# Optimization experiments

Measured on AMD Instinct MI355X. Metric: run time of the kernel, lower is better.

The kernel has to match this reference:

```python
import jax, jax.numpy as jnp
import numpy as np
import math

NUM_HEADS = 16
KEY_SIZE = 64
HIDDEN = 4096
EMBED = 1024
VOCAB = 32000
SEQ = 2048
LAYERS = 4


def rmsnorm(x):
    return x * jax.lax.rsqrt(jnp.mean(x * x, axis=-1, keepdims=True) + 1e-5)


def rope_buffers(seq, d):
    half = d // 2
    i = jnp.arange(d)
    offset = i % half
    scales = jnp.power(10000.0, (-2.0 / d) * offset.astype(jnp.float32))
    m = jnp.arange(seq, dtype=jnp.float32)
    angles = m[:, None] * scales[None, :]  # [S, D]
    cos = jnp.cos(angles)
    sin = jnp.sin(angles)
    sin = jnp.concatenate([-sin[:, :half], sin[:, half:]], axis=-1)
    return cos, sin


def rotate(x, cos, sin):
    # x: [B, H, S, D]; cos/sin: [S, D]
    half = KEY_SIZE // 2
    swapped = jnp.concatenate([x[..., half:], x[..., :half]], axis=-1)
    return cos[None, None] * x + sin[None, None] * swapped


def setup_inputs() -> dict:
    key = jax.random.key(0)
    ks = jax.random.split(key, 7)
    std = 0.02
    return {
        'tokens': jax.random.randint(ks[0], (1, SEQ), 0, VOCAB),
        'table': jax.random.normal(ks[1], (VOCAB, EMBED), jnp.float32) * std,
        'qkv_w': jax.random.normal(ks[2], (LAYERS, EMBED, 3 * NUM_HEADS * KEY_SIZE), jnp.float32) * std,
        'out_w': jax.random.normal(ks[3], (LAYERS, NUM_HEADS * KEY_SIZE, EMBED), jnp.float32) * std,
        'up_w': jax.random.normal(ks[4], (LAYERS, EMBED, 2 * HIDDEN), jnp.float32) * std,
        'down_w': jax.random.normal(ks[5], (LAYERS, HIDDEN, EMBED), jnp.float32) * std,
        'vocab_w': jax.random.normal(ks[6], (EMBED, VOCAB), jnp.float32) * std,
    }


def reference(tokens, table, qkv_w, out_w, up_w, down_w, vocab_w):
    B, S = tokens.shape
    H, D = NUM_HEADS, KEY_SIZE
    # module zeroes embedding row 0 each forward
    table = table.at[0].set(0.0)
    cos, sin = rope_buffers(S, D)
    causal = jnp.tril(jnp.ones((S, S), dtype=bool))  # context_size == S -> pure causal
    emb = table[tokens]  # [B, S, E]
    for l in range(LAYERS):
        # --- self attention ---
        normed = rmsnorm(emb)
        qkv = normed @ qkv_w[l]  # [B, S, 3HD]
        q, k, v = jnp.split(qkv, 3, axis=-1)
        q = q.reshape(B, S, H, D).transpose(0, 2, 1, 3)
        k = k.reshape(B, S, H, D).transpose(0, 2, 1, 3)
        v = v.reshape(B, S, H, D).transpose(0, 2, 1, 3)
        q = rotate(q, cos, sin)
        k = rotate(k, cos, sin)
        attn = jnp.einsum('bhqd,bhkd->bhqk', q, k) / math.sqrt(D)
        attn = jnp.where(causal[None, None], attn, -jnp.inf)
        attn = jax.nn.softmax(attn, axis=-1)
        out = jnp.einsum('bhqk,bhkd->bhqd', attn, v)
        out = out.transpose(0, 2, 1, 3).reshape(B, S, H * D)
        emb = emb + out @ out_w[l]
        # --- SwiGLU FFN ---
        normed = rmsnorm(emb)
        gate_up = normed @ up_w[l]
        gate, up = gate_up[..., :HIDDEN], gate_up[..., HIDDEN:]
        emb = emb + (up * jax.nn.silu(gate)) @ down_w[l]
    emb = rmsnorm(emb)
    logits = emb @ vocab_w  # [B, S, V]
    return logits
```

## Files before the change

### kernel.cpp

```cpp
#include <hip/hip_runtime.h>
#include <hip/hip_bf16.h>

typedef __attribute__((ext_vector_type(8))) short short8;
typedef __attribute__((ext_vector_type(4))) float f32x4;

__device__ __forceinline__ ushort f2bf(float f) {
  uint32_t u = __float_as_uint(f);
  uint32_t r = (u + 0x7FFFu + ((u >> 16) & 1u)) >> 16;
  return (ushort)r;
}
__device__ __forceinline__ float bf2f(ushort u) {
  return __uint_as_float(((uint32_t)u) << 16);
}

__device__ __forceinline__ void gload_lds16(const ushort* g, ushort* l) {
  __builtin_amdgcn_global_load_lds(
      (const __attribute__((address_space(1))) void*)g,
      (__attribute__((address_space(3))) void*)l, 16, 0, 0);
}

__device__ __forceinline__ f32x4 mfma16(short8 a, short8 b, f32x4 c) {
  return __builtin_amdgcn_mfma_f32_16x16x32_bf16(a, b, c, 0, 0, 0);
}

#define BAR() __builtin_amdgcn_s_barrier()
#define WAIT_LGKM()                                        \
  do {                                                     \
    asm volatile("s_waitcnt lgkmcnt(0)" ::: "memory");     \
    __builtin_amdgcn_sched_barrier(0);                     \
  } while (0)
#define WAIT_VM()                                          \
  do {                                                     \
    asm volatile("s_waitcnt vmcnt(0)" ::: "memory");       \
    __builtin_amdgcn_sched_barrier(0);                     \
  } while (0)

__global__ __launch_bounds__(256)
void transpose_conv_kernel(const float* __restrict__ W, ushort* __restrict__ WT,
                           const int K, const int N, const int mode) {
  const size_t lofs = (size_t)blockIdx.z * K * N;
  W += lofs;
  WT += lofs;
  __shared__ float tile[32][33];
  const int n0 = blockIdx.x * 32;
  const int k0 = blockIdx.y * 32;
  const int x = threadIdx.x;
  const int y = threadIdx.y;
#pragma unroll
  for (int j = 0; j < 4; ++j)
    tile[y + j * 8][x] = W[(size_t)(k0 + y + j * 8) * N + n0 + x];
  __syncthreads();
#pragma unroll
  for (int j = 0; j < 4; ++j) {
    int r = n0 + y + j * 8;
    if (mode == 1) r = (r < 4096) ? (2 * r) : (2 * (r - 4096) + 1);
    WT[(size_t)r * K + k0 + x] = f2bf(tile[x][y + j * 8]);
  }
}

__global__ __launch_bounds__(256)
void embed_kernel(const int* __restrict__ tokens, const float* __restrict__ table,
                  float* __restrict__ emb) {
  const int s = blockIdx.x, t = threadIdx.x;
  const int tok = tokens[s];
  float4 v = make_float4(0.f, 0.f, 0.f, 0.f);
  if (tok != 0) v = *(const float4*)&table[(size_t)tok * 1024 + t * 4];
  *(float4*)&emb[(size_t)s * 1024 + t * 4] = v;
}

__global__ __launch_bounds__(256)
void rmsnorm_kernel(const float* __restrict__ x, ushort* __restrict__ out) {
  const int row = blockIdx.x, t = threadIdx.x;
  const float4 v = *(const float4*)&x[(size_t)row * 1024 + t * 4];
  float ss = v.x * v.x + v.y * v.y + v.z * v.z + v.w * v.w;
#pragma unroll
  for (int off = 32; off; off >>= 1) ss += __shfl_xor(ss, off);
  __shared__ float red[4];
  if ((t & 63) == 0) red[t >> 6] = ss;
  __syncthreads();
  const float total = red[0] + red[1] + red[2] + red[3];
  const float sc = rsqrtf(total * (1.f / 1024.f) + 1e-5f);
  ushort4 o;
  o.x = f2bf(v.x * sc); o.y = f2bf(v.y * sc);
  o.z = f2bf(v.z * sc); o.w = f2bf(v.w * sc);
  *(ushort4*)&out[(size_t)row * 1024 + t * 4] = o;
}

__global__ __launch_bounds__(256)
void ropev_kernel(const float* __restrict__ qkv, ushort* __restrict__ qh,
                  ushort* __restrict__ kh, ushort* __restrict__ vt) {
  __shared__ float tv[64][65];
  const int h = blockIdx.y;
  const int s0 = blockIdx.x * 64;
  const int t = threadIdx.x;
#pragma unroll
  for (int j = 0; j < 4; ++j) {
    const int e = j * 1024 + t * 4;
    const int sl = e >> 6, d0 = e & 63;
    const int s = s0 + sl;
    const float* row = qkv + (size_t)s * 3072 + h * 64;
    const float4 xq  = *(const float4*)&row[d0];
    const float4 xqs = *(const float4*)&row[(d0 + 32) & 63];
    const float4 xk  = *(const float4*)&row[1024 + d0];
    const float4 xks = *(const float4*)&row[1024 + ((d0 + 32) & 63)];
    const float4 xv  = *(const float4*)&row[2048 + d0];
    float co[4], si[4];
#pragma unroll
    for (int c = 0; c < 4; ++c) {
      const int d = d0 + c;
      const int off = d & 31;
      const float freq = exp2f(-0.41524101186092029f * (float)off);
      const float ang = (float)s * freq;
      co[c] = cosf(ang);
      const float sv = sinf(ang);
      si[c] = (d < 32) ? -sv : sv;
    }
    ushort4 oq, ok;
    oq.x = f2bf(co[0] * xq.x + si[0] * xqs.x);
    oq.y = f2bf(co[1] * xq.y + si[1] * xqs.y);
    oq.z = f2bf(co[2] * xq.z + si[2] * xqs.z);
    oq.w = f2bf(co[3] * xq.w + si[3] * xqs.w);
    ok.x = f2bf(co[0] * xk.x + si[0] * xks.x);
    ok.y = f2bf(co[1] * xk.y + si[1] * xks.y);
    ok.z = f2bf(co[2] * xk.z + si[2] * xks.z);
    ok.w = f2bf(co[3] * xk.w + si[3] * xks.w);
    const size_t ho = ((size_t)h * 2048 + s) * 64 + d0;
    *(ushort4*)&qh[ho] = oq;
    *(ushort4*)&kh[ho] = ok;
    *(float4*)&tv[sl][d0] = xv;
  }
  __syncthreads();
#pragma unroll
  for (int j = 0; j < 4; ++j) {
    const int e = j * 1024 + t * 4;
    const int d = e >> 6, s4 = e & 63;
    ushort4 ov;
    ov.x = f2bf(tv[s4 + 0][d]);
    ov.y = f2bf(tv[s4 + 1][d]);
    ov.z = f2bf(tv[s4 + 2][d]);
    ov.w = f2bf(tv[s4 + 3][d]);
    *(ushort4*)&vt[((size_t)h * 64 + d) * 2048 + s0 + s4] = ov;
  }
}

__global__ __launch_bounds__(256)
void attn_mfma_kernel(const ushort* __restrict__ qh, const ushort* __restrict__ kh,
                      const ushort* __restrict__ vt, ushort* __restrict__ attn_out) {
  __shared__ ushort sQ[64 * 64];
  __shared__ ushort sK[64 * 64];
  __shared__ ushort sV[64 * 64];
  __shared__ ushort sP[4][1024];
  const int h = blockIdx.y;
  const int bx = blockIdx.x;
  const int qt = (h < 8) ? bx : 31 - bx;
  const int i0 = qt * 64;
  const int tid = threadIdx.x;
  const int w = tid >> 6, lane = tid & 63;
  const int llo = lane & 15, lhi = lane >> 4;
  const int lr = lane >> 3, lc = lane & 7;
  const ushort* qg = qh + ((size_t)h * 2048 + i0) * 64;
  const ushort* kg = kh + (size_t)h * 2048 * 64;
  const ushort* vg = vt + (size_t)h * 64 * 2048;

#pragma unroll
  for (int j = 0; j < 2; ++j) {
    const int r0 = (w * 2 + j) * 8;
    const int row = r0 + lr;
    gload_lds16(qg + (size_t)row * 64 + ((lc ^ (row & 7)) * 8), &sQ[r0 * 64]);
  }
  __syncthreads();
  const int qrow = w * 16 + llo;
  const short8 qf0 = *(const short8*)&sQ[qrow * 64 + ((lhi ^ (qrow & 7)) * 8)];
  const short8 qf1 = *(const short8*)&sQ[qrow * 64 + (((4 + lhi) ^ (qrow & 7)) * 8)];

  float m = -1e30f, lsum = 0.f;
  f32x4 o[4] = {};
  const int nch = qt + 1;
  for (int cb = 0; cb < nch; ++cb) {
    const int kb = cb * 64;
    __syncthreads();
#pragma unroll
    for (int j = 0; j < 2; ++j) {
      const int r0 = (w * 2 + j) * 8;
      const int row = r0 + lr;
      gload_lds16(kg + (size_t)(kb + row) * 64 + ((lc ^ (row & 7)) * 8), &sK[r0 * 64]);
      gload_lds16(vg + (size_t)row * 2048 + kb + ((lc ^ (row & 7)) * 8), &sV[r0 * 64]);
    }
    __syncthreads();

    f32x4 st[4] = {};
#pragma unroll
    for (int ck = 0; ck < 2; ++ck) {
      const short8 qf = ck ? qf1 : qf0;
#pragma unroll
      for (int f = 0; f < 4; ++f) {
        const int key = f * 16 + llo;
        const short8 kf = *(const short8*)&sK[key * 64 + (((ck * 4 + lhi) ^ (key & 7)) * 8)];
        st[f] = mfma16(kf, qf, st[f]);
      }
    }

    float pv[4][4];
    const bool diag = (kb == i0);
#pragma unroll
    for (int f = 0; f < 4; ++f)
#pragma unroll
      for (int r = 0; r < 4; ++r) {
        float x = st[f][r] * 0.125f;
        if (diag && (f * 16 + lhi * 4 + r) > qrow) x = -1e30f;
        pv[f][r] = x;
      }
    float mr = pv[0][0];
#pragma unroll
    for (int f = 0; f < 4; ++f)
#pragma unroll
      for (int r = 0; r < 4; ++r) mr = fmaxf(mr, pv[f][r]);
    mr = fmaxf(mr, __shfl_xor(mr, 16));
    mr = fmaxf(mr, __shfl_xor(mr, 32));
    const float mnew = fmaxf(m, mr);
    const float scale = __expf(m - mnew);
    m = mnew;
    float rs = 0.f;
#pragma unroll
    for (int f = 0; f < 4; ++f)
#pragma unroll
      for (int r = 0; r < 4; ++r) {
        const float p = __expf(pv[f][r] - mnew);
        pv[f][r] = p;
        rs += p;
      }
    rs += __shfl_xor(rs, 16);
    rs += __shfl_xor(rs, 32);
    lsum = lsum * scale + rs;
    float scr[4];
#pragma unroll
    for (int r = 0; r < 4; ++r) scr[r] = __shfl(scale, lhi * 4 + r);
#pragma unroll
    for (int nn = 0; nn < 4; ++nn)
#pragma unroll
      for (int r = 0; r < 4; ++r) o[nn][r] *= scr[r];

    ushort* pw = sP[w];
#pragma unroll
    for (int f = 0; f < 4; ++f) {
      uint2 pk;
      pk.x = (uint)f2bf(pv[f][0]) | ((uint)f2bf(pv[f][1]) << 16);
      pk.y = (uint)f2bf(pv[f][2]) | ((uint)f2bf(pv[f][3]) << 16);
      *(uint2*)&pw[llo * 64 + ((f * 16 + lhi * 4) ^ ((llo & 7) << 3))] = pk;
    }
    const short8 pf0 = *(const short8*)&pw[llo * 64 + ((lhi ^ (llo & 7)) * 8)];
    const short8 pf1 = *(const short8*)&pw[llo * 64 + (((4 + lhi) ^ (llo & 7)) * 8)];

#pragma unroll
    for (int ck = 0; ck < 2; ++ck) {
      const short8 pf = ck ? pf1 : pf0;
#pragma unroll
      for (int nn = 0; nn < 4; ++nn) {
        const int drow = nn * 16 + llo;
        const short8 vf = *(const short8*)&sV[drow * 64 + (((ck * 4 + lhi) ^ (drow & 7)) * 8)];
        o[nn] = mfma16(pf, vf, o[nn]);
      }
    }
  }

  const float inv = 1.f / lsum;
  float invr[4];
#pragma unroll
  for (int r = 0; r < 4; ++r) invr[r] = __shfl(inv, lhi * 4 + r);
#pragma unroll
  for (int nn = 0; nn < 4; ++nn)
#pragma unroll
    for (int r = 0; r < 4; ++r) {
      const int row = i0 + w * 16 + lhi * 4 + r;
      attn_out[(size_t)row * 1024 + h * 64 + nn * 16 + llo] = f2bf(o[nn][r] * invr[r]);
    }
}

template <int BM, int BN, int EPI>
__global__ __launch_bounds__(256)
void gemm_bt_kernel(const ushort* __restrict__ A, const ushort* __restrict__ BT,
                    const float* __restrict__ addend, void* __restrict__ Cout,
                    const int M, const int N, const int K) {
  constexpr int WM = BM / 2, WN = BN / 2;
  constexpr int FM = WM / 16, FN = WN / 16;
  constexpr int CHA = BM / 16, CHB = BN / 16;
  __shared__ ushort sA[BM * 32];
  __shared__ ushort sB[BN * 32];
  const int bm0 = blockIdx.y * BM;
  const int bn0 = blockIdx.x * BN;
  const int tid = threadIdx.x;
  const int wid = tid >> 6;
  const int lane = tid & 63;
  const int wr = wid >> 1, wc = wid & 1;
  const int lhi = lane >> 4, llo = lane & 15;
  f32x4 acc[FM][FN] = {};
  for (int kt = 0; kt < K; kt += 32) {
#pragma unroll
    for (int c2 = 0; c2 < CHA / 4; ++c2) {
      const int ch = c2 * 4 + wid;
      const int e = ch * 512 + lane * 8;
      gload_lds16(A + (size_t)(bm0 + (e >> 5)) * K + kt + (e & 31), sA + ch * 512);
    }
#pragma unroll
    for (int c2 = 0; c2 < CHB / 4; ++c2) {
      const int ch = c2 * 4 + wid;
      const int e = ch * 512 + lane * 8;
      gload_lds16(BT + (size_t)(bn0 + (e >> 5)) * K + kt + (e & 31), sB + ch * 512);
    }
    __syncthreads();
    short8 aF[FM], bF[FN];
#pragma unroll
    for (int mm = 0; mm < FM; ++mm)
      aF[mm] = *(const short8*)&sA[(wr * WM + mm * 16 + llo) * 32 + lhi * 8];
#pragma unroll
    for (int nn = 0; nn < FN; ++nn)
      bF[nn] = *(const short8*)&sB[(wc * WN + nn * 16 + llo) * 32 + lhi * 8];
#pragma unroll
    for (int mm = 0; mm < FM; ++mm)
#pragma unroll
      for (int nn = 0; nn < FN; ++nn)
        acc[mm][nn] = __builtin_amdgcn_mfma_f32_16x16x32_bf16(aF[mm], bF[nn],
                                                              acc[mm][nn], 0, 0, 0);
    __syncthreads();
  }
#pragma unroll
  for (int mm = 0; mm < FM; ++mm) {
#pragma unroll
    for (int nn = 0; nn < FN; ++nn) {
      const int col = bn0 + wc * WN + nn * 16 + llo;
#pragma unroll
      for (int r = 0; r < 4; ++r) {
        const int row = bm0 + wr * WM + mm * 16 + lhi * 4 + r;
        float v = acc[mm][nn][r];
        if constexpr (EPI == 1) v += addend[(size_t)row * N + col];
        ((float*)Cout)[(size_t)row * N + col] = v;
      }
    }
  }
}

#define LDA_(MH)                                                              \
  {                                                                           \
    _Pragma("unroll") for (int mm = 0; mm < 4; ++mm) {                        \
      const int row = wr * 128 + ((MH) * 4 + mm) * 16 + llo;                  \
      _Pragma("unroll") for (int ks = 0; ks < 2; ++ks)                        \
          aF[mm][ks] = *(const short8*)&cA[row * 64 +                         \
                          (((ks * 4 + lhi) ^ (row & 7)) * 8)];                \
    }                                                                         \
  }
#define LDB_(NH)                                                              \
  {                                                                           \
    _Pragma("unroll") for (int nn = 0; nn < 2; ++nn) {                        \
      const int row = wc * 64 + ((NH) * 2 + nn) * 16 + llo;                   \
      _Pragma("unroll") for (int ks = 0; ks < 2; ++ks)                        \
          bF[nn][ks] = *(const short8*)&cB[row * 64 +                         \
                          (((ks * 4 + lhi) ^ (row & 7)) * 8)];                \
    }                                                                         \
  }
#define MFMAQ_(MH, NH)                                                        \
  {                                                                           \
    __builtin_amdgcn_s_setprio(1);                                            \
    _Pragma("unroll") for (int mm = 0; mm < 4; ++mm)                          \
        _Pragma("unroll") for (int nn = 0; nn < 2; ++nn)                      \
            _Pragma("unroll") for (int ks = 0; ks < 2; ++ks)                  \
                acc[(MH) * 4 + mm][(NH) * 2 + nn] =                           \
                    mfma16(aF[mm][ks], bF[nn][ks],                            \
                           acc[(MH) * 4 + mm][(NH) * 2 + nn]);                \
    __builtin_amdgcn_s_setprio(0);                                            \
  }

template <int EPI>
__global__ __launch_bounds__(512, 2)
void gemm8_kernel(const ushort* __restrict__ A, const ushort* __restrict__ BT,
                  void* __restrict__ Cout,
                  const int M, const int N, const int K, const int nby) {
  extern __shared__ ushort smem[];
  const int nwg = gridDim.x;
  const int cpx = nwg >> 3;
  int id = blockIdx.x;
  id = (id & 7) * cpx + (id >> 3);
  const int by = id % nby, bx = id / nby;
  const int bm0 = by * 256, bn0 = bx * 256;
  const int tid = threadIdx.x;
  const int wid = tid >> 6, lane = tid & 63;
  const int wr = wid >> 2, wc = wid & 3;
  const int llo = lane & 15, lhi = lane >> 4;
  const ushort* gA = A + (size_t)bm0 * K;
  const ushort* gB = BT + (size_t)bn0 * K;

  auto stage = [&](const ushort* g, ushort* dst, int kt) {
#pragma unroll
    for (int i = 0; i < 4; ++i) {
      const int chunk = i * 512 + wid * 64 + lane;
      const int row = chunk >> 3, c = chunk & 7;
      gload_lds16(g + (size_t)row * K + kt + ((c ^ (row & 7)) * 8),
                  dst + (size_t)(i * 512 + wid * 64) * 8);
    }
  };

  f32x4 acc[8][4] = {};
  short8 aF[4][2];
  short8 bF[2][2];

  stage(gA, smem, 0);
  stage(gB, smem + 16384, 0);
  WAIT_VM();
  BAR();

  const int nt = K >> 6;
  for (int t = 0; t < nt; ++t) {
    const int cur = t & 1;
    ushort* cA = smem + cur * 32768;
    ushort* cB = cA + 16384;
    ushort* nA = smem + (cur ^ 1) * 32768;
    ushort* nB = nA + 16384;
    const bool pf = (t + 1 < nt);
    LDA_(0); LDB_(0);
    if (pf) { stage(gA, nA, (t + 1) * 64); stage(gB, nB, (t + 1) * 64); }
    BAR(); WAIT_LGKM();
    MFMAQ_(0, 0);
    BAR();
    LDB_(1);
    BAR(); WAIT_LGKM();
    MFMAQ_(0, 1);
    BAR();
    LDA_(1);
    BAR(); WAIT_LGKM();
    MFMAQ_(1, 1);
    BAR();
    LDB_(0);
    BAR(); WAIT_LGKM();
    MFMAQ_(1, 0);
    if (pf) WAIT_VM();
    BAR();
  }

#pragma unroll
  for (int m = 0; m < 8; ++m) {
#pragma unroll
    for (int n = 0; n < 4; ++n) {
      const int col = bn0 + wc * 64 + n * 16 + llo;
#pragma unroll
      for (int r = 0; r < 4; ++r) {
        const int row = bm0 + wr * 128 + m * 16 + lhi * 4 + r;
        float v = acc[m][n][r];
        if constexpr (EPI == 3) {
          const float other = __shfl_xor(v, 1);
          if ((llo & 1) == 0) {
            const float gate = v, up = other;
            const float hh = up * gate / (1.f + expf(-gate));
            ((ushort*)Cout)[(size_t)row * (N >> 1) + (col >> 1)] = f2bf(hh);
          }
        } else {
          ((float*)Cout)[(size_t)row * N + col] = v;
        }
      }
    }
  }
}

extern "C" void kernel_launch(void* const* d_in, const int* in_sizes, int n_in,
                              void* d_out, int out_size, void* d_ws, size_t ws_size,
                              hipStream_t stream) {
  const int* tokens    = (const int*)d_in[0];
  const float* table   = (const float*)d_in[1];
  const float* qkv_w   = (const float*)d_in[2];
  const float* out_w   = (const float*)d_in[3];
  const float* up_w    = (const float*)d_in[4];
  const float* down_w  = (const float*)d_in[5];
  const float* vocab_w = (const float*)d_in[6];
  float* logits = (float*)d_out;

  constexpr int G8_LDS = 131072;
  hipFuncSetAttribute(reinterpret_cast<const void*>(&gemm8_kernel<0>),
                      hipFuncAttributeMaxDynamicSharedMemorySize, G8_LDS);
  hipFuncSetAttribute(reinterpret_cast<const void*>(&gemm8_kernel<3>),
                      hipFuncAttributeMaxDynamicSharedMemorySize, G8_LDS);

  char* p = (char*)d_ws;
  auto alloc = [&](size_t bytes) {
    char* r = p;
    p += (bytes + 255) & ~(size_t)255;
    return r;
  };
  float*  emb    = (float*)alloc(2048ull * 1024 * 4);
  ushort* normed = (ushort*)alloc(2048ull * 1024 * 2);
  float*  qkvbuf = (float*)alloc(2048ull * 3072 * 4);
  ushort* qhb    = (ushort*)alloc(16ull * 2048 * 64 * 2);
  ushort* khb    = (ushort*)alloc(16ull * 2048 * 64 * 2);
  ushort* vtb    = (ushort*)alloc(16ull * 64 * 2048 * 2);
  ushort* attno  = (ushort*)alloc(2048ull * 1024 * 2);
  ushort* hbuf   = (ushort*)alloc(2048ull * 4096 * 2);
  ushort* qkvT   = (ushort*)alloc(4ull * 3072 * 1024 * 2);
  ushort* outT   = (ushort*)alloc(4ull * 1024 * 1024 * 2);
  ushort* upT    = (ushort*)alloc(4ull * 8192 * 1024 * 2);
  ushort* downT  = (ushort*)alloc(4ull * 1024 * 4096 * 2);
  ushort* vocabT = (ushort*)alloc(32000ull * 1024 * 2);

  const dim3 tb(32, 8);
  transpose_conv_kernel<<<dim3(3072 / 32, 1024 / 32, 4), tb, 0, stream>>>(
      qkv_w, qkvT, 1024, 3072, 0);
  transpose_conv_kernel<<<dim3(1024 / 32, 1024 / 32, 4), tb, 0, stream>>>(
      out_w, outT, 1024, 1024, 0);
  transpose_conv_kernel<<<dim3(8192 / 32, 1024 / 32, 4), tb, 0, stream>>>(
      up_w, upT, 1024, 8192, 1);
  transpose_conv_kernel<<<dim3(1024 / 32, 4096 / 32, 4), tb, 0, stream>>>(
      down_w, downT, 4096, 1024, 0);
  transpose_conv_kernel<<<dim3(32000 / 32, 1024 / 32, 1), tb, 0, stream>>>(
      vocab_w, vocabT, 1024, 32000, 0);

  embed_kernel<<<2048, 256, 0, stream>>>(tokens, table, emb);

  for (int l = 0; l < 4; ++l) {
    rmsnorm_kernel<<<2048, 256, 0, stream>>>(emb, normed);
    gemm_bt_kernel<64, 128, 0><<<dim3(3072 / 128, 2048 / 64), 256, 0, stream>>>(
        normed, qkvT + (size_t)l * 3072 * 1024, nullptr, qkvbuf, 2048, 3072, 1024);
    ropev_kernel<<<dim3(32, 16), 256, 0, stream>>>(qkvbuf, qhb, khb, vtb);
    attn_mfma_kernel<<<dim3(32, 16), 256, 0, stream>>>(qhb, khb, vtb, attno);
    gemm_bt_kernel<64, 128, 1><<<dim3(1024 / 128, 2048 / 64), 256, 0, stream>>>(
        attno, outT + (size_t)l * 1024 * 1024, emb, emb, 2048, 1024, 1024);
    rmsnorm_kernel<<<2048, 256, 0, stream>>>(emb, normed);
    gemm8_kernel<3><<<(8192 / 256) * (2048 / 256), 512, G8_LDS, stream>>>(
        normed, upT + (size_t)l * 8192 * 1024, hbuf, 2048, 8192, 1024, 2048 / 256);
    gemm_bt_kernel<64, 128, 1><<<dim3(1024 / 128, 2048 / 64), 256, 0, stream>>>(
        hbuf, downT + (size_t)l * 1024 * 4096, emb, emb, 2048, 1024, 4096);
  }
  rmsnorm_kernel<<<2048, 256, 0, stream>>>(emb, normed);
  gemm8_kernel<0><<<(32000 / 256) * (2048 / 256), 512, G8_LDS, stream>>>(
      normed, vocabT, logits, 2048, 32000, 1024, 2048 / 256);
}
```

Baseline: 1.335 ms.

## Use 256x128 triple-buffered GEMM, route QKV through it, fuse embed with rmsnorm

Replaces the 256x256 double-buffered GEMM with a 256x128 tile that keeps three LDS stages and prefetches two K-steps ahead, waiting only for the older stage's loads (vmcnt(6)). This is meant to hide more global-load latency and double the workgroup count for the up-projection and vocab GEMMs. The QKV projection moves from the small-tile GEMM to this kernel. The first layer's rmsnorm is fused into the embedding kernel to save one launch and one pass over the activations. In exchange, the narrower N tile lowers arithmetic intensity per loaded A tile, and the larger LDS footprint (144 KB) limits residency to one block per CU.

```diff
diff --git a/kernel.cpp b/kernel.cpp
--- a/kernel.cpp
+++ b/kernel.cpp
@@ -29,9 +29,14 @@
     asm volatile("s_waitcnt lgkmcnt(0)" ::: "memory");     \
     __builtin_amdgcn_sched_barrier(0);                     \
   } while (0)
-#define WAIT_VM()                                          \
+#define WAIT_VM0()                                         \
   do {                                                     \
     asm volatile("s_waitcnt vmcnt(0)" ::: "memory");       \
+    __builtin_amdgcn_sched_barrier(0);                     \
+  } while (0)
+#define WAIT_VM6()                                         \
+  do {                                                     \
+    asm volatile("s_waitcnt vmcnt(6)" ::: "memory");       \
     __builtin_amdgcn_sched_barrier(0);                     \
   } while (0)
 
@@ -59,13 +64,25 @@
 }
 
 __global__ __launch_bounds__(256)
-void embed_kernel(const int* __restrict__ tokens, const float* __restrict__ table,
-                  float* __restrict__ emb) {
+void embed_norm_kernel(const int* __restrict__ tokens, const float* __restrict__ table,
+                       float* __restrict__ emb, ushort* __restrict__ normed) {
   const int s = blockIdx.x, t = threadIdx.x;
   const int tok = tokens[s];
   float4 v = make_float4(0.f, 0.f, 0.f, 0.f);
   if (tok != 0) v = *(const float4*)&table[(size_t)tok * 1024 + t * 4];
   *(float4*)&emb[(size_t)s * 1024 + t * 4] = v;
+  float ss = v.x * v.x + v.y * v.y + v.z * v.z + v.w * v.w;
+#pragma unroll
+  for (int off = 32; off; off >>= 1) ss += __shfl_xor(ss, off);
+  __shared__ float red[4];
+  if ((t & 63) == 0) red[t >> 6] = ss;
+  __syncthreads();
+  const float total = red[0] + red[1] + red[2] + red[3];
+  const float sc = rsqrtf(total * (1.f / 1024.f) + 1e-5f);
+  ushort4 o;
+  o.x = f2bf(v.x * sc); o.y = f2bf(v.y * sc);
+  o.z = f2bf(v.z * sc); o.w = f2bf(v.w * sc);
+  *(ushort4*)&normed[(size_t)s * 1024 + t * 4] = o;
 }
 
 __global__ __launch_bounds__(256)
@@ -339,48 +356,18 @@
   }
 }
 
-#define LDA_(MH)                                                              \
-  {                                                                           \
-    _Pragma("unroll") for (int mm = 0; mm < 4; ++mm) {                        \
-      const int row = wr * 128 + ((MH) * 4 + mm) * 16 + llo;                  \
-      _Pragma("unroll") for (int ks = 0; ks < 2; ++ks)                        \
-          aF[mm][ks] = *(const short8*)&cA[row * 64 +                         \
-                          (((ks * 4 + lhi) ^ (row & 7)) * 8)];                \
-    }                                                                         \
-  }
-#define LDB_(NH)                                                              \
-  {                                                                           \
-    _Pragma("unroll") for (int nn = 0; nn < 2; ++nn) {                        \
-      const int row = wc * 64 + ((NH) * 2 + nn) * 16 + llo;                   \
-      _Pragma("unroll") for (int ks = 0; ks < 2; ++ks)                        \
-          bF[nn][ks] = *(const short8*)&cB[row * 64 +                         \
-                          (((ks * 4 + lhi) ^ (row & 7)) * 8)];                \
-    }                                                                         \
-  }
-#define MFMAQ_(MH, NH)                                                        \
-  {                                                                           \
-    __builtin_amdgcn_s_setprio(1);                                            \
-    _Pragma("unroll") for (int mm = 0; mm < 4; ++mm)                          \
-        _Pragma("unroll") for (int nn = 0; nn < 2; ++nn)                      \
-            _Pragma("unroll") for (int ks = 0; ks < 2; ++ks)                  \
-                acc[(MH) * 4 + mm][(NH) * 2 + nn] =                           \
-                    mfma16(aF[mm][ks], bF[nn][ks],                            \
-                           acc[(MH) * 4 + mm][(NH) * 2 + nn]);                \
-    __builtin_amdgcn_s_setprio(0);                                            \
-  }
-
 template <int EPI>
 __global__ __launch_bounds__(512, 2)
-void gemm8_kernel(const ushort* __restrict__ A, const ushort* __restrict__ BT,
-                  void* __restrict__ Cout,
-                  const int M, const int N, const int K, const int nby) {
+void gemm8b_kernel(const ushort* __restrict__ A, const ushort* __restrict__ BT,
+                   void* __restrict__ Cout,
+                   const int M, const int N, const int K, const int nby) {
   extern __shared__ ushort smem[];
   const int nwg = gridDim.x;
   const int cpx = nwg >> 3;
   int id = blockIdx.x;
   id = (id & 7) * cpx + (id >> 3);
   const int by = id % nby, bx = id / nby;
-  const int bm0 = by * 256, bn0 = bx * 256;
+  const int bm0 = by * 256, bn0 = bx * 128;
   const int tid = threadIdx.x;
   const int wid = tid >> 6, lane = tid & 63;
   const int wr = wid >> 2, wc = wid & 3;
@@ -388,58 +375,90 @@
   const ushort* gA = A + (size_t)bm0 * K;
   const ushort* gB = BT + (size_t)bn0 * K;
 
-  auto stage = [&](const ushort* g, ushort* dst, int kt) {
+  auto stage = [&](ushort* dst, int kt) {
 #pragma unroll
     for (int i = 0; i < 4; ++i) {
       const int chunk = i * 512 + wid * 64 + lane;
       const int row = chunk >> 3, c = chunk & 7;
-      gload_lds16(g + (size_t)row * K + kt + ((c ^ (row & 7)) * 8),
+      gload_lds16(gA + (size_t)row * K + kt + ((c ^ (row & 7)) * 8),
                   dst + (size_t)(i * 512 + wid * 64) * 8);
     }
+#pragma unroll
+    for (int i = 0; i < 2; ++i) {
+      const int chunk = i * 512 + wid * 64 + lane;
+      const int row = chunk >> 3, c = chunk & 7;
+      gload_lds16(gB + (size_t)row * K + kt + ((c ^ (row & 7)) * 8),
+                  dst + 16384 + (size_t)(i * 512 + wid * 64) * 8);
+    }
   };
 
-  f32x4 acc[8][4] = {};
-  short8 aF[4][2];
-  short8 bF[2][2];
-
-  stage(gA, smem, 0);
-  stage(gB, smem + 16384, 0);
-  WAIT_VM();
+  f32x4 acc[8][2] = {};
+  short8 aF[8][2];
+  short8 bF[2];
+
+  const int nt = K >> 6;
+  stage(smem, 0);
+  if (nt > 1) {
+    stage(smem + 24576, 64);
+    WAIT_VM6();
+  } else {
+    WAIT_VM0();
+  }
   BAR();
 
-  const int nt = K >> 6;
+  int cs = 0;
   for (int t = 0; t < nt; ++t) {
-    const int cur = t & 1;
-    ushort* cA = smem + cur * 32768;
+    ushort* cA = smem + cs * 24576;
     ushort* cB = cA + 16384;
-    ushort* nA = smem + (cur ^ 1) * 32768;
-    ushort* nB = nA + 16384;
-    const bool pf = (t + 1 < nt);
-    LDA_(0); LDB_(0);
-    if (pf) { stage(gA, nA, (t + 1) * 64); stage(gB, nB, (t + 1) * 64); }
+    int ss = cs + 2; if (ss >= 3) ss -= 3;
+    const bool pf2 = (t + 2 < nt);
+    if (pf2) stage(smem + ss * 24576, (t + 2) * 64);
+#pragma unroll
+    for (int mm = 0; mm < 8; ++mm) {
+      const int row = wr * 128 + mm * 16 + llo;
+#pragma unroll
+      for (int ks = 0; ks < 2; ++ks)
+        aF[mm][ks] = *(const short8*)&cA[row * 64 + (((ks * 4 + lhi) ^ (row & 7)) * 8)];
+    }
+    {
+      const int row = wc * 32 + llo;
+#pragma unroll
+      for (int ks = 0; ks < 2; ++ks)
+        bF[ks] = *(const short8*)&cB[row * 64 + (((ks * 4 + lhi) ^ (row & 7)) * 8)];
+    }
     BAR(); WAIT_LGKM();
-    MFMAQ_(0, 0);
+    __builtin_amdgcn_s_setprio(1);
+#pragma unroll
+    for (int mm = 0; mm < 8; ++mm)
+#pragma unroll
+      for (int ks = 0; ks < 2; ++ks)
+        acc[mm][0] = mfma16(aF[mm][ks], bF[ks], acc[mm][0]);
+    __builtin_amdgcn_s_setprio(0);
     BAR();
-    LDB_(1);
+    {
+      const int row = wc * 32 + 16 + llo;
+#pragma unroll
+      for (int ks = 0; ks < 2; ++ks)
+        bF[ks] = *(const short8*)&cB[row * 64 + (((ks * 4 + lhi) ^ (row & 7)) * 8)];
+    }
     BAR(); WAIT_LGKM();
-    MFMAQ_(0, 1);
+    __builtin_amdgcn_s_setprio(1);
+#pragma unroll
+    for (int mm = 0; mm < 8; ++mm)
+#pragma unroll
+      for (int ks = 0; ks < 2; ++ks)
+        acc[mm][1] = mfma16(aF[mm][ks], bF[ks], acc[mm][1]);
+    __builtin_amdgcn_s_setprio(0);
+    if (pf2) { WAIT_VM6(); } else { WAIT_VM0(); }
     BAR();
-    LDA_(1);
-    BAR(); WAIT_LGKM();
-    MFMAQ_(1, 1);
-    BAR();
-    LDB_(0);
-    BAR(); WAIT_LGKM();
-    MFMAQ_(1, 0);
-    if (pf) WAIT_VM();
-    BAR();
+    ++cs; if (cs == 3) cs = 0;
   }
 
 #pragma unroll
   for (int m = 0; m < 8; ++m) {
 #pragma unroll
-    for (int n = 0; n < 4; ++n) {
-      const int col = bn0 + wc * 64 + n * 16 + llo;
+    for (int n = 0; n < 2; ++n) {
+      const int col = bn0 + wc * 32 + n * 16 + llo;
 #pragma unroll
       for (int r = 0; r < 4; ++r) {
         const int row = bm0 + wr * 128 + m * 16 + lhi * 4 + r;
@@ -471,10 +490,10 @@
   const float* vocab_w = (const float*)d_in[6];
   float* logits = (float*)d_out;
 
-  constexpr int G8_LDS = 131072;
-  hipFuncSetAttribute(reinterpret_cast<const void*>(&gemm8_kernel<0>),
+  constexpr int G8_LDS = 147456;
+  hipFuncSetAttribute(reinterpret_cast<const void*>(&gemm8b_kernel<0>),
                       hipFuncAttributeMaxDynamicSharedMemorySize, G8_LDS);
-  hipFuncSetAttribute(reinterpret_cast<const void*>(&gemm8_kernel<3>),
+  hipFuncSetAttribute(reinterpret_cast<const void*>(&gemm8b_kernel<3>),
                       hipFuncAttributeMaxDynamicSharedMemorySize, G8_LDS);
 
   char* p = (char*)d_ws;
@@ -509,23 +528,23 @@
   transpose_conv_kernel<<<dim3(32000 / 32, 1024 / 32, 1), tb, 0, stream>>>(
       vocab_w, vocabT, 1024, 32000, 0);
 
-  embed_kernel<<<2048, 256, 0, stream>>>(tokens, table, emb);
+  embed_norm_kernel<<<2048, 256, 0, stream>>>(tokens, table, emb, normed);
 
   for (int l = 0; l < 4; ++l) {
-    rmsnorm_kernel<<<2048, 256, 0, stream>>>(emb, normed);
-    gemm_bt_kernel<64, 128, 0><<<dim3(3072 / 128, 2048 / 64), 256, 0, stream>>>(
-        normed, qkvT + (size_t)l * 3072 * 1024, nullptr, qkvbuf, 2048, 3072, 1024);
+    if (l > 0) rmsnorm_kernel<<<2048, 256, 0, stream>>>(emb, normed);
+    gemm8b_kernel<0><<<(3072 / 128) * (2048 / 256), 512, G8_LDS, stream>>>(
+        normed, qkvT + (size_t)l * 3072 * 1024, qkvbuf, 2048, 3072, 1024, 2048 / 256);
     ropev_kernel<<<dim3(32, 16), 256, 0, stream>>>(qkvbuf, qhb, khb, vtb);
     attn_mfma_kernel<<<dim3(32, 16), 256, 0, stream>>>(qhb, khb, vtb, attno);
     gemm_bt_kernel<64, 128, 1><<<dim3(1024 / 128, 2048 / 64), 256, 0, stream>>>(
         attno, outT + (size_t)l * 1024 * 1024, emb, emb, 2048, 1024, 1024);
     rmsnorm_kernel<<<2048, 256, 0, stream>>>(emb, normed);
-    gemm8_kernel<3><<<(8192 / 256) * (2048 / 256), 512, G8_LDS, stream>>>(
+    gemm8b_kernel<3><<<(8192 / 128) * (2048 / 256), 512, G8_LDS, stream>>>(
         normed, upT + (size_t)l * 8192 * 1024, hbuf, 2048, 8192, 1024, 2048 / 256);
     gemm_bt_kernel<64, 128, 1><<<dim3(1024 / 128, 2048 / 64), 256, 0, stream>>>(
         hbuf, downT + (size_t)l * 1024 * 4096, emb, emb, 2048, 1024, 4096);
   }
   rmsnorm_kernel<<<2048, 256, 0, stream>>>(emb, normed);
-  gemm8_kernel<0><<<(32000 / 256) * (2048 / 256), 512, G8_LDS, stream>>>(
+  gemm8b_kernel<0><<<(32000 / 128) * (2048 / 256), 512, G8_LDS, stream>>>(
       normed, vocabT, logits, 2048, 32000, 1024, 2048 / 256);
 }
```

Measured after the change: 1.333 ms. Within noise of the previous version (-0.1%).

## Fuse RoPE into QKV GEMM epilogue and widen weight-transpose tiles

Applied to the files above, without the earlier changes.

The QKV GEMM now applies rotary embedding in its epilogue, using a precomputed cos/sin table, and writes bf16 Q/K/V in per-head layout directly. This removes the fp32 qkv buffer round trip and the per-element transcendental math in the old rope kernel. A small kernel now only transposes V. Separately, the first layer's rmsnorm is fused into the embedding kernel, and the weight transpose-convert kernel uses 64x64 tiles with vectorized float4 loads and ushort4 stores. The epilogue stores are scattered 2-byte writes, which may be less coalesced.

```diff
diff --git a/kernel.cpp b/kernel.cpp
--- a/kernel.cpp
+++ b/kernel.cpp
@@ -29,7 +29,7 @@
     asm volatile("s_waitcnt lgkmcnt(0)" ::: "memory");     \
     __builtin_amdgcn_sched_barrier(0);                     \
   } while (0)
-#define WAIT_VM()                                          \
+#define WAIT_VM0()                                         \
   do {                                                     \
     asm volatile("s_waitcnt vmcnt(0)" ::: "memory");       \
     __builtin_amdgcn_sched_barrier(0);                     \
@@ -41,31 +41,61 @@
   const size_t lofs = (size_t)blockIdx.z * K * N;
   W += lofs;
   WT += lofs;
-  __shared__ float tile[32][33];
-  const int n0 = blockIdx.x * 32;
-  const int k0 = blockIdx.y * 32;
-  const int x = threadIdx.x;
-  const int y = threadIdx.y;
-#pragma unroll
-  for (int j = 0; j < 4; ++j)
-    tile[y + j * 8][x] = W[(size_t)(k0 + y + j * 8) * N + n0 + x];
+  __shared__ float tile[64][65];
+  const int n0 = blockIdx.x * 64;
+  const int k0 = blockIdx.y * 64;
+  const int t = threadIdx.x;
+#pragma unroll
+  for (int j = 0; j < 4; ++j) {
+    const int idx = j * 1024 + t * 4;
+    const int kk = idx >> 6, nn = idx & 63;
+    *(float4*)&tile[kk][nn] = *(const float4*)&W[(size_t)(k0 + kk) * N + n0 + nn];
+  }
   __syncthreads();
 #pragma unroll
   for (int j = 0; j < 4; ++j) {
-    int r = n0 + y + j * 8;
-    if (mode == 1) r = (r < 4096) ? (2 * r) : (2 * (r - 4096) + 1);
-    WT[(size_t)r * K + k0 + x] = f2bf(tile[x][y + j * 8]);
-  }
-}
-
-__global__ __launch_bounds__(256)
-void embed_kernel(const int* __restrict__ tokens, const float* __restrict__ table,
-                  float* __restrict__ emb) {
+    const int idx = j * 1024 + t * 4;
+    const int nn = idx >> 6, kk = idx & 63;
+    int rr = n0 + nn;
+    if (mode == 1) rr = (rr < 4096) ? (2 * rr) : (2 * (rr - 4096) + 1);
+    ushort4 o;
+    o.x = f2bf(tile[kk + 0][nn]);
+    o.y = f2bf(tile[kk + 1][nn]);
+    o.z = f2bf(tile[kk + 2][nn]);
+    o.w = f2bf(tile[kk + 3][nn]);
+    *(ushort4*)&WT[(size_t)rr * K + k0 + kk] = o;
+  }
+}
+
+__global__ __launch_bounds__(256)
+void sincos_kernel(float2* __restrict__ cstab) {
+  const int idx = blockIdx.x * 256 + threadIdx.x;
+  const int s = idx >> 5, o = idx & 31;
+  const float freq = exp2f(-0.41524101186092029f * (float)o);
+  const float a = (float)s * freq;
+  cstab[idx] = make_float2(cosf(a), sinf(a));
+}
+
+__global__ __launch_bounds__(256)
+void embed_norm_kernel(const int* __restrict__ tokens, const float* __restrict__ table,
+                       float* __restrict__ emb, ushort* __restrict__ normed) {
   const int s = blockIdx.x, t = threadIdx.x;
   const int tok = tokens[s];
   float4 v = make_float4(0.f, 0.f, 0.f, 0.f);
   if (tok != 0) v = *(const float4*)&table[(size_t)tok * 1024 + t * 4];
   *(float4*)&emb[(size_t)s * 1024 + t * 4] = v;
+  float ss = v.x * v.x + v.y * v.y + v.z * v.z + v.w * v.w;
+#pragma unroll
+  for (int off = 32; off; off >>= 1) ss += __shfl_xor(ss, off);
+  __shared__ float red[4];
+  if ((t & 63) == 0) red[t >> 6] = ss;
+  __syncthreads();
+  const float total = red[0] + red[1] + red[2] + red[3];
+  const float sc = rsqrtf(total * (1.f / 1024.f) + 1e-5f);
+  ushort4 o;
+  o.x = f2bf(v.x * sc); o.y = f2bf(v.y * sc);
+  o.z = f2bf(v.z * sc); o.w = f2bf(v.w * sc);
+  *(ushort4*)&normed[(size_t)s * 1024 + t * 4] = o;
 }
 
 __global__ __launch_bounds__(256)
@@ -87,58 +117,27 @@
 }
 
 __global__ __launch_bounds__(256)
-void ropev_kernel(const float* __restrict__ qkv, ushort* __restrict__ qh,
-                  ushort* __restrict__ kh, ushort* __restrict__ vt) {
-  __shared__ float tv[64][65];
+void vtrans_kernel(const ushort* __restrict__ vh, ushort* __restrict__ vt) {
+  __shared__ ushort tv[64][68];
   const int h = blockIdx.y;
   const int s0 = blockIdx.x * 64;
   const int t = threadIdx.x;
 #pragma unroll
   for (int j = 0; j < 4; ++j) {
-    const int e = j * 1024 + t * 4;
-    const int sl = e >> 6, d0 = e & 63;
-    const int s = s0 + sl;
-    const float* row = qkv + (size_t)s * 3072 + h * 64;
-    const float4 xq  = *(const float4*)&row[d0];
-    const float4 xqs = *(const float4*)&row[(d0 + 32) & 63];
-    const float4 xk  = *(const float4*)&row[1024 + d0];
-    const float4 xks = *(const float4*)&row[1024 + ((d0 + 32) & 63)];
-    const float4 xv  = *(const float4*)&row[2048 + d0];
-    float co[4], si[4];
-#pragma unroll
-    for (int c = 0; c < 4; ++c) {
-      const int d = d0 + c;
-      const int off = d & 31;
-      const float freq = exp2f(-0.41524101186092029f * (float)off);
-      const float ang = (float)s * freq;
-      co[c] = cosf(ang);
-      const float sv = sinf(ang);
-      si[c] = (d < 32) ? -sv : sv;
-    }
-    ushort4 oq, ok;
-    oq.x = f2bf(co[0] * xq.x + si[0] * xqs.x);
-    oq.y = f2bf(co[1] * xq.y + si[1] * xqs.y);
-    oq.z = f2bf(co[2] * xq.z + si[2] * xqs.z);
-    oq.w = f2bf(co[3] * xq.w + si[3] * xqs.w);
-    ok.x = f2bf(co[0] * xk.x + si[0] * xks.x);
-    ok.y = f2bf(co[1] * xk.y + si[1] * xks.y);
-    ok.z = f2bf(co[2] * xk.z + si[2] * xks.z);
-    ok.w = f2bf(co[3] * xk.w + si[3] * xks.w);
-    const size_t ho = ((size_t)h * 2048 + s) * 64 + d0;
-    *(ushort4*)&qh[ho] = oq;
-    *(ushort4*)&kh[ho] = ok;
-    *(float4*)&tv[sl][d0] = xv;
+    const int idx = j * 1024 + t * 4;
+    const int s = idx >> 6, d4 = idx & 63;
+    *(ushort4*)&tv[s][d4] = *(const ushort4*)&vh[((size_t)h * 2048 + s0 + s) * 64 + d4];
   }
   __syncthreads();
 #pragma unroll
   for (int j = 0; j < 4; ++j) {
-    const int e = j * 1024 + t * 4;
-    const int d = e >> 6, s4 = e & 63;
+    const int idx = j * 1024 + t * 4;
+    const int d = idx >> 6, s4 = idx & 63;
     ushort4 ov;
-    ov.x = f2bf(tv[s4 + 0][d]);
-    ov.y = f2bf(tv[s4 + 1][d]);
-    ov.z = f2bf(tv[s4 + 2][d]);
-    ov.w = f2bf(tv[s4 + 3][d]);
+    ov.x = tv[s4 + 0][d];
+    ov.y = tv[s4 + 1][d];
+    ov.z = tv[s4 + 2][d];
+    ov.w = tv[s4 + 3][d];
     *(ushort4*)&vt[((size_t)h * 64 + d) * 2048 + s0 + s4] = ov;
   }
 }
@@ -334,6 +333,79 @@
         float v = acc[mm][nn][r];
         if constexpr (EPI == 1) v += addend[(size_t)row * N + col];
         ((float*)Cout)[(size_t)row * N + col] = v;
+      }
+    }
+  }
+}
+
+__global__ __launch_bounds__(256)
+void gemm_qkv_kernel(const ushort* __restrict__ A, const ushort* __restrict__ BT,
+                     const float2* __restrict__ cstab, ushort* __restrict__ qh,
+                     ushort* __restrict__ kh, ushort* __restrict__ vh, const int K) {
+  constexpr int BM = 64, BN = 128, WM = 32, WN = 64, FM = 2, FN = 4;
+  constexpr int CHA = BM / 16, CHB = BN / 16;
+  __shared__ ushort sA[BM * 32];
+  __shared__ ushort sB[BN * 32];
+  const int bm0 = blockIdx.y * BM;
+  const int bn0 = blockIdx.x * BN;
+  const int tid = threadIdx.x;
+  const int wid = tid >> 6;
+  const int lane = tid & 63;
+  const int wr = wid >> 1, wc = wid & 1;
+  const int lhi = lane >> 4, llo = lane & 15;
+  f32x4 acc[FM][FN] = {};
+  for (int kt = 0; kt < K; kt += 32) {
+#pragma unroll
+    for (int c2 = 0; c2 < CHA / 4; ++c2) {
+      const int ch = c2 * 4 + wid;
+      const int e = ch * 512 + lane * 8;
+      gload_lds16(A + (size_t)(bm0 + (e >> 5)) * K + kt + (e & 31), sA + ch * 512);
+    }
+#pragma unroll
+    for (int c2 = 0; c2 < CHB / 4; ++c2) {
+      const int ch = c2 * 4 + wid;
+      const int e = ch * 512 + lane * 8;
+      gload_lds16(BT + (size_t)(bn0 + (e >> 5)) * K + kt + (e & 31), sB + ch * 512);
+    }
+    __syncthreads();
+    short8 aF[FM], bF[FN];
+#pragma unroll
+    for (int mm = 0; mm < FM; ++mm)
+      aF[mm] = *(const short8*)&sA[(wr * WM + mm * 16 + llo) * 32 + lhi * 8];
+#pragma unroll
+    for (int nn = 0; nn < FN; ++nn)
+      bF[nn] = *(const short8*)&sB[(wc * WN + nn * 16 + llo) * 32 + lhi * 8];
+#pragma unroll
+    for (int mm = 0; mm < FM; ++mm)
+#pragma unroll
+      for (int nn = 0; nn < FN; ++nn)
+        acc[mm][nn] = mfma16(aF[mm], bF[nn], acc[mm][nn]);
+    __syncthreads();
+  }
+#pragma unroll
+  for (int mm = 0; mm < FM; ++mm) {
+#pragma unroll
+    for (int nn = 0; nn < FN; ++nn) {
+      const int col = bn0 + wc * WN + nn * 16 + llo;
+      const int part = col >> 10;
+      const int hcol = col & 1023;
+      const int h = hcol >> 6;
+      const int d = hcol & 63;
+      const int off = d & 31;
+#pragma unroll
+      for (int r = 0; r < 4; ++r) {
+        const int row = bm0 + wr * WM + mm * 16 + lhi * 4 + r;
+        const float v = acc[mm][nn][r];
+        const size_t ho = ((size_t)h * 2048 + row) * 64 + d;
+        if (part == 2) {
+          vh[ho] = f2bf(v);
+        } else {
+          const float pt = acc[mm][nn ^ 2][r];
+          const float2 cn = cstab[row * 32 + off];
+          const float si = (d < 32) ? -cn.y : cn.y;
+          const ushort o = f2bf(cn.x * v + si * pt);
+          if (part == 0) qh[ho] = o; else kh[ho] = o;
+        }
       }
     }
   }
@@ -404,7 +476,7 @@
 
   stage(gA, smem, 0);
   stage(gB, smem + 16384, 0);
-  WAIT_VM();
+  WAIT_VM0();
   BAR();
 
   const int nt = K >> 6;
@@ -431,7 +503,7 @@
     LDB_(0);
     BAR(); WAIT_LGKM();
     MFMAQ_(1, 0);
-    if (pf) WAIT_VM();
+    if (pf) WAIT_VM0();
     BAR();
   }
 
@@ -485,9 +557,10 @@
   };
   float*  emb    = (float*)alloc(2048ull * 1024 * 4);
   ushort* normed = (ushort*)alloc(2048ull * 1024 * 2);
-  float*  qkvbuf = (float*)alloc(2048ull * 3072 * 4);
+  float2* cstab  = (float2*)alloc(2048ull * 32 * 8);
   ushort* qhb    = (ushort*)alloc(16ull * 2048 * 64 * 2);
   ushort* khb    = (ushort*)alloc(16ull * 2048 * 64 * 2);
+  ushort* vhb    = (ushort*)alloc(16ull * 2048 * 64 * 2);
   ushort* vtb    = (ushort*)alloc(16ull * 64 * 2048 * 2);
   ushort* attno  = (ushort*)alloc(2048ull * 1024 * 2);
   ushort* hbuf   = (ushort*)alloc(2048ull * 4096 * 2);
@@ -497,25 +570,25 @@
   ushort* downT  = (ushort*)alloc(4ull * 1024 * 4096 * 2);
   ushort* vocabT = (ushort*)alloc(32000ull * 1024 * 2);
 
-  const dim3 tb(32, 8);
-  transpose_conv_kernel<<<dim3(3072 / 32, 1024 / 32, 4), tb, 0, stream>>>(
+  transpose_conv_kernel<<<dim3(3072 / 64, 1024 / 64, 4), 256, 0, stream>>>(
       qkv_w, qkvT, 1024, 3072, 0);
-  transpose_conv_kernel<<<dim3(1024 / 32, 1024 / 32, 4), tb, 0, stream>>>(
+  transpose_conv_kernel<<<dim3(1024 / 64, 1024 / 64, 4), 256, 0, stream>>>(
       out_w, outT, 1024, 1024, 0);
-  transpose_conv_kernel<<<dim3(8192 / 32, 1024 / 32, 4), tb, 0, stream>>>(
+  transpose_conv_kernel<<<dim3(8192 / 64, 1024 / 64, 4), 256, 0, stream>>>(
       up_w, upT, 1024, 8192, 1);
-  transpose_conv_kernel<<<dim3(1024 / 32, 4096 / 32, 4), tb, 0, stream>>>(
+  transpose_conv_kernel<<<dim3(1024 / 64, 4096 / 64, 4), 256, 0, stream>>>(
       down_w, downT, 4096, 1024, 0);
-  transpose_conv_kernel<<<dim3(32000 / 32, 1024 / 32, 1), tb, 0, stream>>>(
+  transpose_conv_kernel<<<dim3(32000 / 64, 1024 / 64, 1), 256, 0, stream>>>(
       vocab_w, vocabT, 1024, 32000, 0);
-
-  embed_kernel<<<2048, 256, 0, stream>>>(tokens, table, emb);
+  sincos_kernel<<<256, 256, 0, stream>>>(cstab);
+
+  embed_norm_kernel<<<2048, 256, 0, stream>>>(tokens, table, emb, normed);
 
   for (int l = 0; l < 4; ++l) {
-    rmsnorm_kernel<<<2048, 256, 0, stream>>>(emb, normed);
-    gemm_bt_kernel<64, 128, 0><<<dim3(3072 / 128, 2048 / 64), 256, 0, stream>>>(
-        normed, qkvT + (size_t)l * 3072 * 1024, nullptr, qkvbuf, 2048, 3072, 1024);
-    ropev_kernel<<<dim3(32, 16), 256, 0, stream>>>(qkvbuf, qhb, khb, vtb);
+    if (l > 0) rmsnorm_kernel<<<2048, 256, 0, stream>>>(emb, normed);
+    gemm_qkv_kernel<<<dim3(3072 / 128, 2048 / 64), 256, 0, stream>>>(
+        normed, qkvT + (size_t)l * 3072 * 1024, cstab, qhb, khb, vhb, 1024);
+    vtrans_kernel<<<dim3(32, 16), 256, 0, stream>>>(vhb, vtb);
     attn_mfma_kernel<<<dim3(32, 16), 256, 0, stream>>>(qhb, khb, vtb, attno);
     gemm_bt_kernel<64, 128, 1><<<dim3(1024 / 128, 2048 / 64), 256, 0, stream>>>(
         attno, outT + (size_t)l * 1024 * 1024, emb, emb, 2048, 1024, 1024);
```

Measured after the change: 1.316 ms. No clear change (-1.4%).
